# Kernel tuning notes

Measured on AMD Instinct MI355X. Metric: run time of the kernel, lower is better.

## Reference

```python
import jax, jax.numpy as jnp
import numpy as np
import math

GAUSSIAN_KERNEL = 3.0  # sigma from init_kwargs


def setup_inputs() -> dict:
    key = jax.random.key(0)
    k1, k2, k3, k4 = jax.random.split(key, 4)
    B, De, Do, T, H, W = 4, 128, 512, 10, 32, 32
    return {
        "m_in": jax.random.normal(k1, (B, De, T, H, W), dtype=jnp.float32),
        "m_out": jax.random.normal(k2, (B, Do, T, H, W), dtype=jnp.float32),
        "q_in": jax.random.normal(k3, (B, De, H, W), dtype=jnp.float32),
        "q_out": jax.random.normal(k4, (B, Do, H, W), dtype=jnp.float32),
    }


def _gaussian_kernel_map(corr, H, W, sigma):
    # corr: [B, THW, HW]; for each memory location, gaussian centered at its
    # argmax query position over the HxW query grid.
    idx = jnp.argmax(corr, axis=2)                       # [B, THW] int
    idx_y = (idx // W).astype(corr.dtype)[..., None, None]  # [B, THW, 1, 1]
    idx_x = (idx % W).astype(corr.dtype)[..., None, None]
    y = jnp.arange(H, dtype=corr.dtype).reshape(1, 1, H, 1)
    x = jnp.arange(W, dtype=corr.dtype).reshape(1, 1, 1, W)
    g = jnp.exp(-((x - idx_x) ** 2 + (y - idx_y) ** 2) / (2.0 * sigma ** 2))
    return g.reshape(corr.shape)                         # [B, THW, HW]


def reference(m_in, m_out, q_in, q_out):
    B, De, T, H, W = m_in.shape
    Do = m_out.shape[1]
    THW, HW = T * H * W, H * W

    mi = m_in.reshape(B, De, THW)       # [B, De, THW]
    qi = q_in.reshape(B, De, HW)        # [B, De, HW]
    # p[b, t, q] = <memory key t, query key q> / sqrt(De)
    p = jnp.einsum('bdt,bdq->btq', mi, qi) / math.sqrt(De)   # [B, THW, HW]

    gauss = _gaussian_kernel_map(p, H, W, GAUSSIAN_KERNEL)

    # softmax over memory dimension (dim=1), then gaussian reweight + renorm
    p_soft = jax.nn.softmax(p, axis=1)
    p_w = p_soft * gauss
    p_w = p_w / jnp.sum(p_w, axis=1, keepdims=True)

    mo = m_out.reshape(B, Do, THW)
    mem = jnp.einsum('bdt,btq->bdq', mo, p_w).reshape(B, Do, H, W)
    mem_out = jnp.concatenate([mem, q_out], axis=1)      # [B, 2*Do, H, W]
    return mem_out, p_w
```

## Files before the change

kernel.cpp:

```cpp
#include <hip/hip_runtime.h>
#include <hip/hip_bf16.h>

#define BB 4
#define DE 128
#define DO_ 512
#define THW 10240
#define HW 1024
#define SCALE 0.08838834764831845f
#define INV2S2 0.05555555555555555f
#define NCH 32
#define CHT 320

#define WS_PART_F  81920
#define WS_STATS_F 344064
#define WS_MO16_B  1409024ull
#define WS_PWT_B   43352064ull
#define WS_MITH_B  (WS_PWT_B)
#define WS_MITL_B  (WS_PWT_B + 10485760ull)
#define WS_QITH_B  (WS_PWT_B + 20971520ull)
#define WS_QITL_B  (WS_PWT_B + 22020096ull)

using bf16x8 = __attribute__((ext_vector_type(8))) short;
using f16x8  = __attribute__((ext_vector_type(8))) _Float16;
using f32x4  = __attribute__((ext_vector_type(4))) float;
using u16x8  = __attribute__((ext_vector_type(8))) unsigned short;

__device__ __forceinline__ unsigned short f2bf(float f) {
    __hip_bfloat16 h = __float2bfloat16(f);
    return *reinterpret_cast<unsigned short*>(&h);
}
__device__ __forceinline__ void glds16(const void* g, void* l) {
    __builtin_amdgcn_global_load_lds((const __attribute__((address_space(1))) void*)g,
                                     (__attribute__((address_space(3))) void*)l,
                                     16, 0, 0);
}
__device__ __forceinline__ unsigned int ordf(float f) {
    unsigned int u = __float_as_uint(f);
    return (u & 0x80000000u) ? ~u : (u | 0x80000000u);
}

__global__ __launch_bounds__(256) void k_init(float* __restrict__ out,
                                              const float* __restrict__ qout,
                                              float4* __restrict__ amax4)
{
    int idx = blockIdx.x * 256 + threadIdx.x;
    if (idx < 20480) amax4[idx] = make_float4(0.f, 0.f, 0.f, 0.f);
    int b  = idx >> 18;
    int r  = idx & 262143;
    int c  = r >> 8;
    int q4 = r & 255;
    float4* dst = (float4*)out + idx;
    if (c < DO_) {
        *dst = make_float4(0.f, 0.f, 0.f, 0.f);
    } else {
        const float4* src = (const float4*)qout + ((size_t)(b * DO_ + (c - DO_)) << 8) + q4;
        *dst = *src;
    }
}

__global__ __launch_bounds__(256) void k_split(const float* __restrict__ src,
                                               unsigned short* __restrict__ dstH,
                                               unsigned short* __restrict__ dstL,
                                               int ncols, float scale)
{
    __shared__ float tile[128][65];
    int t0 = blockIdx.x * 64;
    int b  = blockIdx.z;
    int tid = threadIdx.x;
    const float* S = src + (size_t)b * DE * ncols + t0;
#pragma unroll
    for (int i = 0; i < 8; ++i) {
        int s  = tid + i * 256;
        int k  = s >> 4;
        int c4 = (s & 15) << 2;
        *(float4*)&tile[k][c4] = *(const float4*)&S[(size_t)k * ncols + c4];
    }
    __syncthreads();
#pragma unroll
    for (int i = 0; i < 4; ++i) {
        int s  = tid + i * 256;
        int t  = s >> 4;
        int k8 = s & 15;
        u16x8 oh, ol;
#pragma unroll
        for (int j = 0; j < 8; ++j) {
            float v = tile[k8 * 8 + j][t] * scale;
            _Float16 h = (_Float16)v;
            float rr = v - (float)h;
            _Float16 l = (_Float16)(rr * 2048.0f);
            oh[j] = *(unsigned short*)&h;
            ol[j] = *(unsigned short*)&l;
        }
        size_t o = ((size_t)b * ncols + t0 + t) * 128 + k8 * 8;
        *(u16x8*)&dstH[o] = oh;
        *(u16x8*)&dstL[o] = ol;
    }
}

__global__ __launch_bounds__(256) void k_gemm1m(const unsigned short* __restrict__ AH,
                                                const unsigned short* __restrict__ AL,
                                                const unsigned short* __restrict__ BH,
                                                const unsigned short* __restrict__ BL,
                                                float* __restrict__ p,
                                                unsigned long long* __restrict__ amax)
{
    __shared__ unsigned short AsH[2][4096];
    __shared__ unsigned short AsL[2][4096];
    __shared__ unsigned short BsH[2][4096];
    __shared__ unsigned short BsL[2][4096];
    int id  = blockIdx.x;
    int tbg = id & 7;
    int rr  = id >> 3;
    int b   = rr / 80;
    int j   = rr - b * 80;
    int tb  = tbg * 10 + (j >> 3);
    int qb  = j & 7;
    int tid = threadIdx.x;
    int w = tid >> 6, lane = tid & 63;
    int quad = lane >> 4, l15 = lane & 15;

    const char* AgH = (const char*)AH + ((size_t)b * THW + (size_t)tb * 128) * 256;
    const char* AgL = (const char*)AL + ((size_t)b * THW + (size_t)tb * 128) * 256;
    const char* BgH = (const char*)BH + ((size_t)b * HW + qb * 128) * 256;
    const char* BgL = (const char*)BL + ((size_t)b * HW + qb * 128) * 256;

    int srow = lane >> 2;
    int sj   = (lane & 3) ^ (srow & 3);
    size_t ro0 = (size_t)(w * 32 + srow) * 256 + sj * 16;
    size_t ro1 = (size_t)(w * 32 + 16 + srow) * 256 + sj * 16;

#define G1_STAGE(BUF, KB) do {                                                          \
    char* _d;                                                                           \
    _d = (char*)AsH + (BUF) * 8192 + w * 2048;                                          \
    glds16(AgH + ro0 + (KB), _d); glds16(AgH + ro1 + (KB), _d + 1024);                  \
    _d = (char*)AsL + (BUF) * 8192 + w * 2048;                                          \
    glds16(AgL + ro0 + (KB), _d); glds16(AgL + ro1 + (KB), _d + 1024);                  \
    _d = (char*)BsH + (BUF) * 8192 + w * 2048;                                          \
    glds16(BgH + ro0 + (KB), _d); glds16(BgH + ro1 + (KB), _d + 1024);                  \
    _d = (char*)BsL + (BUF) * 8192 + w * 2048;                                          \
    glds16(BgL + ro0 + (KB), _d); glds16(BgL + ro1 + (KB), _d + 1024);                  \
  } while (0)

    int wm = w >> 1, wn = w & 1;
    int fq = ((l15 & 3) ^ quad) << 4;
    const char* aFH = (const char*)AsH + (wm * 64 + l15) * 64 + fq;
    const char* aFL = (const char*)AsL + (wm * 64 + l15) * 64 + fq;
    const char* bFH = (const char*)BsH + (wn * 64 + l15) * 64 + fq;
    const char* bFL = (const char*)BsL + (wn * 64 + l15) * 64 + fq;

    f32x4 acc1[4][4], acc2[4][4];
#pragma unroll
    for (int i = 0; i < 4; ++i)
#pragma unroll
        for (int j2 = 0; j2 < 4; ++j2) {
            acc1[i][j2] = (f32x4){0.f, 0.f, 0.f, 0.f};
            acc2[i][j2] = (f32x4){0.f, 0.f, 0.f, 0.f};
        }

    G1_STAGE(0, 0);
    int cur = 0;
    for (int kc = 0; kc < 4; ++kc) {
        if (kc < 3) {
            G1_STAGE(cur ^ 1, (size_t)(kc + 1) * 64);
            asm volatile("s_waitcnt vmcnt(8)" ::: "memory");
        } else {
            asm volatile("s_waitcnt vmcnt(0)" ::: "memory");
        }
        __builtin_amdgcn_s_barrier();
        __builtin_amdgcn_sched_barrier(0);
        int cb = cur * 8192;
        f16x8 afH[4], afL[4], bfH[4], bfL[4];
#pragma unroll
        for (int i = 0; i < 4; ++i) {
            afH[i] = *(const f16x8*)(aFH + cb + i * 1024);
            afL[i] = *(const f16x8*)(aFL + cb + i * 1024);
            bfH[i] = *(const f16x8*)(bFH + cb + i * 1024);
            bfL[i] = *(const f16x8*)(bFL + cb + i * 1024);
        }
#pragma unroll
        for (int i = 0; i < 4; ++i)
#pragma unroll
            for (int j2 = 0; j2 < 4; ++j2)
                acc1[i][j2] = __builtin_amdgcn_mfma_f32_16x16x32_f16(afH[i], bfH[j2], acc1[i][j2], 0, 0, 0);
#pragma unroll
        for (int i = 0; i < 4; ++i)
#pragma unroll
            for (int j2 = 0; j2 < 4; ++j2)
                acc2[i][j2] = __builtin_amdgcn_mfma_f32_16x16x32_f16(afH[i], bfL[j2], acc2[i][j2], 0, 0, 0);
#pragma unroll
        for (int i = 0; i < 4; ++i)
#pragma unroll
            for (int j2 = 0; j2 < 4; ++j2)
                acc2[i][j2] = __builtin_amdgcn_mfma_f32_16x16x32_f16(afL[i], bfH[j2], acc2[i][j2], 0, 0, 0);
        __builtin_amdgcn_sched_barrier(0);
        __builtin_amdgcn_s_barrier();
        cur ^= 1;
    }
#undef G1_STAGE

    const float inv2048 = 4.8828125e-4f;
    int t0 = tb * 128 + wm * 64;
    float* Pg = p + ((size_t)b * THW + t0) * HW + qb * 128 + wn * 64;
    int qbase = qb * 128 + wn * 64;
#pragma unroll
    for (int i = 0; i < 4; ++i) {
#pragma unroll
        for (int r = 0; r < 4; ++r) {
            int tl = i * 16 + quad * 4 + r;
            float v[4];
#pragma unroll
            for (int j2 = 0; j2 < 4; ++j2) {
                v[j2] = acc1[i][j2][r] + acc2[i][j2][r] * inv2048;
                Pg[(size_t)tl * HW + j2 * 16 + l15] = v[j2];
            }
            float best = v[0]; int bj = 0;
#pragma unroll
            for (int j2 = 1; j2 < 4; ++j2)
                if (v[j2] > best) { best = v[j2]; bj = j2; }
            int q = qbase + bj * 16 + l15;
            unsigned long long pk = ((unsigned long long)ordf(best) << 32)
                                  | (unsigned long long)(0xFFFFFFFFu - (unsigned)q);
#pragma unroll
            for (int off = 1; off < 16; off <<= 1) {
                unsigned long long o = __shfl_xor(pk, off);
                if (o > pk) pk = o;
            }
            if (l15 == 0)
                atomicMax(&amax[(size_t)b * THW + t0 + tl], pk);
        }
    }
}

__global__ __launch_bounds__(256) void k_colstats(const float* __restrict__ p,
                                                  const unsigned long long* __restrict__ amax,
                                                  float* __restrict__ part)
{
    int q  = blockIdx.x * 256 + threadIdx.x;
    int ch = blockIdx.y, b = blockIdx.z;
    float x = (float)(q & 31), y = (float)(q >> 5);
    const float* pp = p + ((size_t)b * THW + ch * CHT) * HW + q;
    const unsigned long long* am = amax + (size_t)b * THW + ch * CHT;
    float m = -3.0e38f, s = 0.f;
    for (int i = 0; i < CHT; ++i) {
        unsigned idx = 0xFFFFFFFFu - (unsigned)am[i];
        float dx = x - (float)(idx & 31), dy = y - (float)(idx >> 5);
        float z = pp[(size_t)i * HW] - (dx * dx + dy * dy) * INV2S2;
        float nm = fmaxf(m, z);
        s = s * __expf(m - nm) + __expf(z - nm);
        m = nm;
    }
    size_t o = ((size_t)(b * NCH + ch) * HW + q) * 2;
    part[o] = m; part[o + 1] = s;
}

__global__ __launch_bounds__(256) void k_reduce(const float* __restrict__ part,
                                                float* __restrict__ stats)
{
    int i = blockIdx.x * 256 + threadIdx.x;
    int b = i >> 10, q = i & 1023;
    float M = -3.0e38f;
#pragma unroll
    for (int c = 0; c < NCH; ++c)
        M = fmaxf(M, part[((size_t)(b * NCH + c) * HW + q) * 2]);
    float S = 0.f;
#pragma unroll
    for (int c = 0; c < NCH; ++c) {
        size_t o = ((size_t)(b * NCH + c) * HW + q) * 2;
        S += part[o + 1] * __expf(part[o] - M);
    }
    stats[(size_t)i * 2] = M;
    stats[(size_t)i * 2 + 1] = 1.0f / S;
}

__global__ __launch_bounds__(256) void k_pwt(float* __restrict__ p,
                                             const unsigned long long* __restrict__ amax,
                                             const float* __restrict__ stats,
                                             unsigned short* __restrict__ pwT)
{
    __shared__ float tile[64][65];
    __shared__ float ctr[128];
    __shared__ float st[128];
    int qb = blockIdx.x, tb = blockIdx.y, b = blockIdx.z;
    int tid = threadIdx.x;
    if (tid < 64) {
        unsigned idx = 0xFFFFFFFFu - (unsigned)amax[(size_t)b * THW + tb * 64 + tid];
        ctr[tid * 2]     = (float)(idx & 31);
        ctr[tid * 2 + 1] = (float)(idx >> 5);
    }
    if (tid < 128)
        st[tid] = stats[((size_t)b * HW + qb * 64) * 2 + tid];
    __syncthreads();
    int r0 = tid >> 4;
    int c4 = (tid & 15) << 2;
#pragma unroll
    for (int i = 0; i < 4; ++i) {
        int r = r0 + i * 16;
        float* pp = p + ((size_t)b * THW + tb * 64 + r) * HW + qb * 64 + c4;
        float4 v = *(float4*)pp;
        float cx = ctr[r * 2], cy = ctr[r * 2 + 1];
        float vv[4] = {v.x, v.y, v.z, v.w};
#pragma unroll
        for (int j = 0; j < 4; ++j) {
            int q = qb * 64 + c4 + j;
            float x = (float)(q & 31), y = (float)(q >> 5);
            float dx = x - cx, dy = y - cy;
            vv[j] = __expf(vv[j] - (dx * dx + dy * dy) * INV2S2 - st[(c4 + j) * 2])
                    * st[(c4 + j) * 2 + 1];
            tile[r][c4 + j] = vv[j];
        }
        *(float4*)pp = make_float4(vv[0], vv[1], vv[2], vv[3]);
    }
    __syncthreads();
    int ql = tid >> 3;
    int t0 = (tid & 7) << 3;
#pragma unroll
    for (int pass = 0; pass < 2; ++pass) {
        int q = ql + pass * 32;
        u16x8 o8;
#pragma unroll
        for (int j = 0; j < 8; ++j)
            o8[j] = f2bf(tile[t0 + j][q]);
        *(u16x8*)&pwT[((size_t)b * HW + qb * 64 + q) * THW + tb * 64 + t0] = o8;
    }
}

__global__ __launch_bounds__(256) void k_mo16(const float* __restrict__ mo,
                                              unsigned short* __restrict__ o)
{
    size_t base = ((size_t)blockIdx.x * 256 + threadIdx.x) * 8;
    float4 a = *(const float4*)(mo + base);
    float4 c = *(const float4*)(mo + base + 4);
    u16x8 v;
    v[0] = f2bf(a.x); v[1] = f2bf(a.y); v[2] = f2bf(a.z); v[3] = f2bf(a.w);
    v[4] = f2bf(c.x); v[5] = f2bf(c.y); v[6] = f2bf(c.z); v[7] = f2bf(c.w);
    *(u16x8*)(o + base) = v;
}

__global__ __launch_bounds__(256) void k_gemm2m(const unsigned short* __restrict__ A16,
                                                const unsigned short* __restrict__ B16,
                                                float* __restrict__ out)
{
    __shared__ unsigned short As[2][4096];
    __shared__ unsigned short Bs[2][4096];
    int id   = blockIdx.x;
    int xcd  = id & 7;
    int rest = id >> 3;
    int shi  = rest >> 5;
    int jj   = rest & 31;
    int s    = xcd + (shi << 3);
    int b    = s >> 3, ks = s & 7;
    int mb   = jj >> 3, nb = jj & 7;
    int tid = threadIdx.x;
    int w = tid >> 6, lane = tid & 63;
    int quad = lane >> 4, l15 = lane & 15;

    const char* Ag = (const char*)(A16 + (size_t)b * DO_ * THW + (size_t)mb * 128 * THW + ks * 1280);
    const char* Bg = (const char*)(B16 + (size_t)b * HW * THW + (size_t)nb * 128 * THW + ks * 1280);

    int srow = lane >> 2;
    int sj   = (lane & 3) ^ (srow & 3);
    const char* aP0 = Ag + (size_t)((w * 2 + 0) * 16 + srow) * (THW * 2) + sj * 16;
    const char* aP1 = Ag + (size_t)((w * 2 + 1) * 16 + srow) * (THW * 2) + sj * 16;
    const char* bP0 = Bg + (size_t)((w * 2 + 0) * 16 + srow) * (THW * 2) + sj * 16;
    const char* bP1 = Bg + (size_t)((w * 2 + 1) * 16 + srow) * (THW * 2) + sj * 16;
    char* lA0 = (char*)As + (w * 2 + 0) * 1024;
    char* lA1 = (char*)As + (w * 2 + 1) * 1024;
    char* lB0 = (char*)Bs + (w * 2 + 0) * 1024;
    char* lB1 = (char*)Bs + (w * 2 + 1) * 1024;

#define G2_STAGE(BUF, KB) do {                          \
    glds16(aP0 + (KB), lA0 + (BUF) * 8192);             \
    glds16(aP1 + (KB), lA1 + (BUF) * 8192);             \
    glds16(bP0 + (KB), lB0 + (BUF) * 8192);             \
    glds16(bP1 + (KB), lB1 + (BUF) * 8192);             \
  } while (0)

    int wm = w >> 1, wn = w & 1;
    int fq = ((l15 & 3) ^ quad) << 4;
    const char* aF = (const char*)As + (wm * 64 + l15) * 64 + fq;
    const char* bF = (const char*)Bs + (wn * 64 + l15) * 64 + fq;

    f32x4 acc[4][4];
#pragma unroll
    for (int i = 0; i < 4; ++i)
#pragma unroll
        for (int j = 0; j < 4; ++j)
            acc[i][j] = (f32x4){0.f, 0.f, 0.f, 0.f};

    G2_STAGE(0, 0);
    int cur = 0;
    for (int kit = 0; kit < 40; ++kit) {
        if (kit < 39) {
            G2_STAGE(cur ^ 1, (size_t)(kit + 1) * 64);
            asm volatile("s_waitcnt vmcnt(4)" ::: "memory");
        } else {
            asm volatile("s_waitcnt vmcnt(0)" ::: "memory");
        }
        __builtin_amdgcn_s_barrier();
        __builtin_amdgcn_sched_barrier(0);
        int cb = cur * 8192;
        bf16x8 af[4], bfr[4];
#pragma unroll
        for (int i = 0; i < 4; ++i) af[i]  = *(const bf16x8*)(aF + cb + i * 1024);
#pragma unroll
        for (int j = 0; j < 4; ++j) bfr[j] = *(const bf16x8*)(bF + cb + j * 1024);
#pragma unroll
        for (int i = 0; i < 4; ++i)
#pragma unroll
            for (int j = 0; j < 4; ++j)
                acc[i][j] = __builtin_amdgcn_mfma_f32_16x16x32_bf16(af[i], bfr[j], acc[i][j], 0, 0, 0);
        __builtin_amdgcn_sched_barrier(0);
        __builtin_amdgcn_s_barrier();
        cur ^= 1;
    }
#undef G2_STAGE

    float* Cg = out + (size_t)b * (2 * DO_ * HW);
    int d0 = mb * 128 + wm * 64 + quad * 4;
    int q0 = nb * 128 + wn * 64 + l15;
#pragma unroll
    for (int i = 0; i < 4; ++i)
#pragma unroll
        for (int j = 0; j < 4; ++j)
#pragma unroll
            for (int r = 0; r < 4; ++r)
                atomicAdd(&Cg[(size_t)(d0 + i * 16 + r) * HW + q0 + j * 16], acc[i][j][r]);
}

extern "C" void kernel_launch(void* const* d_in, const int* in_sizes, int n_in,
                              void* d_out, int out_size, void* d_ws, size_t ws_size,
                              hipStream_t stream)
{
    const float* m_in  = (const float*)d_in[0];
    const float* m_out = (const float*)d_in[1];
    const float* q_in  = (const float*)d_in[2];
    const float* q_out = (const float*)d_in[3];
    float* out = (float*)d_out;
    float* pw  = out + (size_t)BB * 2 * DO_ * HW;
    float* ws  = (float*)d_ws;
    unsigned long long* amax = (unsigned long long*)d_ws;
    float* part    = ws + WS_PART_F;
    float* stats   = ws + WS_STATS_F;
    unsigned short* mo16  = (unsigned short*)((char*)d_ws + WS_MO16_B);
    unsigned short* pwT16 = (unsigned short*)((char*)d_ws + WS_PWT_B);
    unsigned short* miTH  = (unsigned short*)((char*)d_ws + WS_MITH_B);
    unsigned short* miTL  = (unsigned short*)((char*)d_ws + WS_MITL_B);
    unsigned short* qiTH  = (unsigned short*)((char*)d_ws + WS_QITH_B);
    unsigned short* qiTL  = (unsigned short*)((char*)d_ws + WS_QITL_B);

    hipLaunchKernelGGL(k_init,    dim3(4096),        dim3(256), 0, stream, out, q_out, (float4*)d_ws);
    hipLaunchKernelGGL(k_split,   dim3(160, 1, BB),  dim3(256), 0, stream, m_in, miTH, miTL, THW, 1.0f);
    hipLaunchKernelGGL(k_split,   dim3(16, 1, BB),   dim3(256), 0, stream, q_in, qiTH, qiTL, HW, SCALE);
    hipLaunchKernelGGL(k_gemm1m,  dim3(2560),        dim3(256), 0, stream, miTH, miTL, qiTH, qiTL, pw, amax);
    hipLaunchKernelGGL(k_colstats,dim3(4, NCH, BB),  dim3(256), 0, stream, pw, amax, part);
    hipLaunchKernelGGL(k_reduce,  dim3(16),          dim3(256), 0, stream, part, stats);
    hipLaunchKernelGGL(k_mo16,    dim3(10240),       dim3(256), 0, stream, m_out, mo16);
    hipLaunchKernelGGL(k_pwt,     dim3(16, 160, BB), dim3(256), 0, stream, pw, amax, stats, pwT16);
    hipLaunchKernelGGL(k_gemm2m,  dim3(1024),        dim3(256), 0, stream, mo16, pwT16, out);
}
```

Baseline: 517.8 us.

## Drop split-K in second GEMM, use 128x64 tiles with direct stores

The output GEMM previously split the K dimension (THW) into 8 slices across 1024 blocks and combined the 128x128 partial tiles with atomicAdd. It now runs 256 blocks, each covering the full K range for a 128x64 output tile with 128-wide K steps, XOR-swizzled LDS, and plain stores. This removes the atomic traffic and the partial-sum contention, and makes the init pass's zeroing of that region unnecessary. The cost is less parallelism: 256 blocks each looping 160 K-iterations, which may underfill the GPU's compute units and lengthen each block's serial path.

```diff
diff --git a/kernel.cpp b/kernel.cpp
--- a/kernel.cpp
+++ b/kernel.cpp
@@ -340,75 +340,93 @@
                                                 const unsigned short* __restrict__ B16,
                                                 float* __restrict__ out)
 {
-    __shared__ unsigned short As[2][4096];
+    __shared__ unsigned short As[2][8192];
     __shared__ unsigned short Bs[2][4096];
-    int id   = blockIdx.x;
-    int xcd  = id & 7;
-    int rest = id >> 3;
-    int shi  = rest >> 5;
-    int jj   = rest & 31;
-    int s    = xcd + (shi << 3);
-    int b    = s >> 3, ks = s & 7;
-    int mb   = jj >> 3, nb = jj & 7;
+    int id  = blockIdx.x;
+    int xcd = id & 7;
+    int j   = id >> 3;
+    int pair = xcd * 2 + (j >> 4);
+    int b  = pair >> 2, mb = pair & 3;
+    int nb = j & 15;
     int tid = threadIdx.x;
     int w = tid >> 6, lane = tid & 63;
     int quad = lane >> 4, l15 = lane & 15;
 
-    const char* Ag = (const char*)(A16 + (size_t)b * DO_ * THW + (size_t)mb * 128 * THW + ks * 1280);
-    const char* Bg = (const char*)(B16 + (size_t)b * HW * THW + (size_t)nb * 128 * THW + ks * 1280);
-
-    int srow = lane >> 2;
-    int sj   = (lane & 3) ^ (srow & 3);
-    const char* aP0 = Ag + (size_t)((w * 2 + 0) * 16 + srow) * (THW * 2) + sj * 16;
-    const char* aP1 = Ag + (size_t)((w * 2 + 1) * 16 + srow) * (THW * 2) + sj * 16;
-    const char* bP0 = Bg + (size_t)((w * 2 + 0) * 16 + srow) * (THW * 2) + sj * 16;
-    const char* bP1 = Bg + (size_t)((w * 2 + 1) * 16 + srow) * (THW * 2) + sj * 16;
-    char* lA0 = (char*)As + (w * 2 + 0) * 1024;
-    char* lA1 = (char*)As + (w * 2 + 1) * 1024;
-    char* lB0 = (char*)Bs + (w * 2 + 0) * 1024;
-    char* lB1 = (char*)Bs + (w * 2 + 1) * 1024;
-
-#define G2_STAGE(BUF, KB) do {                          \
-    glds16(aP0 + (KB), lA0 + (BUF) * 8192);             \
-    glds16(aP1 + (KB), lA1 + (BUF) * 8192);             \
-    glds16(bP0 + (KB), lB0 + (BUF) * 8192);             \
-    glds16(bP1 + (KB), lB1 + (BUF) * 8192);             \
+    const char* Ag = (const char*)(A16 + ((size_t)b * DO_ + mb * 128) * THW);
+    const char* Bg = (const char*)(B16 + ((size_t)b * HW + nb * 64) * THW);
+
+    int lrow = lane >> 3;
+    int lg   = lane & 7;
+    const char* aP[4]; int aO[4];
+    const char* bP[2]; int bO[2];
+#pragma unroll
+    for (int c = 0; c < 4; ++c) {
+        int sr = w * 32 + c * 8 + lrow;
+        aP[c] = Ag + (size_t)sr * (THW * 2) + ((lg ^ (sr & 7)) * 16);
+        aO[c] = (w * 32 + c * 8) * 128;
+    }
+#pragma unroll
+    for (int c = 0; c < 2; ++c) {
+        int sr = w * 16 + c * 8 + lrow;
+        bP[c] = Bg + (size_t)sr * (THW * 2) + ((lg ^ (sr & 7)) * 16);
+        bO[c] = (w * 16 + c * 8) * 128;
+    }
+
+#define G2_STAGE(BUF, KB) do {                                         \
+    glds16(aP[0] + (KB), (char*)As + (BUF) * 16384 + aO[0]);           \
+    glds16(aP[1] + (KB), (char*)As + (BUF) * 16384 + aO[1]);           \
+    glds16(aP[2] + (KB), (char*)As + (BUF) * 16384 + aO[2]);           \
+    glds16(aP[3] + (KB), (char*)As + (BUF) * 16384 + aO[3]);           \
+    glds16(bP[0] + (KB), (char*)Bs + (BUF) * 8192  + bO[0]);           \
+    glds16(bP[1] + (KB), (char*)Bs + (BUF) * 8192  + bO[1]);           \
   } while (0)
 
     int wm = w >> 1, wn = w & 1;
-    int fq = ((l15 & 3) ^ quad) << 4;
-    const char* aF = (const char*)As + (wm * 64 + l15) * 64 + fq;
-    const char* bF = (const char*)Bs + (wn * 64 + l15) * 64 + fq;
-
-    f32x4 acc[4][4];
+    int slot0 = (quad ^ (l15 & 7)) * 16;
+    int slot1 = ((4 + quad) ^ (l15 & 7)) * 16;
+    const char* aF = (const char*)As + (wm * 64 + l15) * 128;
+    const char* bF = (const char*)Bs + (wn * 32 + l15) * 128;
+
+    f32x4 acc[4][2];
 #pragma unroll
     for (int i = 0; i < 4; ++i)
 #pragma unroll
-        for (int j = 0; j < 4; ++j)
-            acc[i][j] = (f32x4){0.f, 0.f, 0.f, 0.f};
+        for (int jj = 0; jj < 2; ++jj)
+            acc[i][jj] = (f32x4){0.f, 0.f, 0.f, 0.f};
 
     G2_STAGE(0, 0);
     int cur = 0;
-    for (int kit = 0; kit < 40; ++kit) {
-        if (kit < 39) {
-            G2_STAGE(cur ^ 1, (size_t)(kit + 1) * 64);
-            asm volatile("s_waitcnt vmcnt(4)" ::: "memory");
+    for (int kit = 0; kit < 160; ++kit) {
+        if (kit < 159) {
+            G2_STAGE(cur ^ 1, (size_t)(kit + 1) * 128);
+            asm volatile("s_waitcnt vmcnt(6)" ::: "memory");
         } else {
             asm volatile("s_waitcnt vmcnt(0)" ::: "memory");
         }
         __builtin_amdgcn_s_barrier();
         __builtin_amdgcn_sched_barrier(0);
-        int cb = cur * 8192;
-        bf16x8 af[4], bfr[4];
-#pragma unroll
-        for (int i = 0; i < 4; ++i) af[i]  = *(const bf16x8*)(aF + cb + i * 1024);
-#pragma unroll
-        for (int j = 0; j < 4; ++j) bfr[j] = *(const bf16x8*)(bF + cb + j * 1024);
+        int ca = cur * 16384, cb2 = cur * 8192;
+        bf16x8 af0[4], af1[4], bf0[2], bf1[2];
+#pragma unroll
+        for (int i = 0; i < 4; ++i) {
+            af0[i] = *(const bf16x8*)(aF + ca + i * 2048 + slot0);
+            af1[i] = *(const bf16x8*)(aF + ca + i * 2048 + slot1);
+        }
+#pragma unroll
+        for (int jj = 0; jj < 2; ++jj) {
+            bf0[jj] = *(const bf16x8*)(bF + cb2 + jj * 2048 + slot0);
+            bf1[jj] = *(const bf16x8*)(bF + cb2 + jj * 2048 + slot1);
+        }
 #pragma unroll
         for (int i = 0; i < 4; ++i)
 #pragma unroll
-            for (int j = 0; j < 4; ++j)
-                acc[i][j] = __builtin_amdgcn_mfma_f32_16x16x32_bf16(af[i], bfr[j], acc[i][j], 0, 0, 0);
+            for (int jj = 0; jj < 2; ++jj)
+                acc[i][jj] = __builtin_amdgcn_mfma_f32_16x16x32_bf16(af0[i], bf0[jj], acc[i][jj], 0, 0, 0);
+#pragma unroll
+        for (int i = 0; i < 4; ++i)
+#pragma unroll
+            for (int jj = 0; jj < 2; ++jj)
+                acc[i][jj] = __builtin_amdgcn_mfma_f32_16x16x32_bf16(af1[i], bf1[jj], acc[i][jj], 0, 0, 0);
         __builtin_amdgcn_sched_barrier(0);
         __builtin_amdgcn_s_barrier();
         cur ^= 1;
@@ -417,14 +435,14 @@
 
     float* Cg = out + (size_t)b * (2 * DO_ * HW);
     int d0 = mb * 128 + wm * 64 + quad * 4;
-    int q0 = nb * 128 + wn * 64 + l15;
+    int q0 = nb * 64 + wn * 32 + l15;
 #pragma unroll
     for (int i = 0; i < 4; ++i)
 #pragma unroll
-        for (int j = 0; j < 4; ++j)
+        for (int jj = 0; jj < 2; ++jj)
 #pragma unroll
             for (int r = 0; r < 4; ++r)
-                atomicAdd(&Cg[(size_t)(d0 + i * 16 + r) * HW + q0 + j * 16], acc[i][j][r]);
+                Cg[(size_t)(d0 + i * 16 + r) * HW + q0 + jj * 16] = acc[i][jj][r];
 }
 
 extern "C" void kernel_launch(void* const* d_in, const int* in_sizes, int n_in,
@@ -456,5 +474,5 @@
     hipLaunchKernelGGL(k_reduce,  dim3(16),          dim3(256), 0, stream, part, stats);
     hipLaunchKernelGGL(k_mo16,    dim3(10240),       dim3(256), 0, stream, m_out, mo16);
     hipLaunchKernelGGL(k_pwt,     dim3(16, 160, BB), dim3(256), 0, stream, pw, amax, stats, pwT16);
-    hipLaunchKernelGGL(k_gemm2m,  dim3(1024),        dim3(256), 0, stream, mo16, pwT16, out);
-}
+    hipLaunchKernelGGL(k_gemm2m,  dim3(256),         dim3(256), 0, stream, mo16, pwT16, out);
+}
```

Result: slower. 590.8 us (+14.1%).
